# Kernel optimization log

Measured on AMD Instinct MI355X. Metric: run time of the kernel, lower is better.

The kernel has to match this reference:

```python
import jax, jax.numpy as jnp
import numpy as np

EPS = 1e-5
NUM_PIXELS = 2  # M_Relax window half-width


def _conv(x, w, b, groups=1, pad=0):
    y = jax.lax.conv_general_dilated(
        x, w, (1, 1), [(pad, pad), (pad, pad)],
        dimension_numbers=("NCHW", "OIHW", "NCHW"),
        feature_group_count=groups)
    return y + b[None, :, None, None]


def _bn(x, g, bta, m, v):
    # eval-mode BatchNorm2d with running stats
    inv = jax.lax.rsqrt(v + EPS)
    return g[None, :, None, None] * (x - m[None, :, None, None]) * inv[None, :, None, None] + bta[None, :, None, None]


def _resb(x, w1, b1, w2, b2):
    y = _conv(x, w1, b1, groups=4, pad=1)
    y = jnp.where(y > 0, y, 0.1 * y)  # LeakyReLU(0.1)
    y = _conv(y, w2, b2, groups=4, pad=1)
    return y + x


def _relax(M):
    # M: (N, w, w); sum of shifts +-NUM_PIXELS along the row (dim 1)
    w = M.shape[1]
    P = jnp.pad(M, ((0, 0), (NUM_PIXELS, NUM_PIXELS), (0, 0)))
    out = P[:, 0:w, :]
    for k in range(1, 2 * NUM_PIXELS + 1):
        out = out + P[:, k:k + w, :]
    return out


def setup_inputs() -> dict:
    key = jax.random.key(0)
    ks = jax.random.split(key, 16)
    b, c, h, w = 4, 64, 128, 256
    c2 = 2 * c
    s = 0.05
    inp = {
        "x_left": jax.random.normal(ks[0], (b, c, h, w), jnp.float32),
        "x_right": jax.random.normal(ks[1], (b, c, h, w), jnp.float32),
        "conv1_w": jax.random.normal(ks[2], (c, c, 1, 1), jnp.float32) * s,
        "conv1_b": jnp.zeros((c,), jnp.float32),
        "conv2_w": jax.random.normal(ks[3], (c, c, 1, 1), jnp.float32) * s,
        "conv2_b": jnp.zeros((c,), jnp.float32),
        "bn_g": jnp.ones((c2,), jnp.float32),
        "bn_b": jnp.zeros((c2,), jnp.float32),
        "bn_m": jax.random.normal(ks[4], (c2,), jnp.float32) * 0.1,
        "bn_v": jax.random.uniform(ks[5], (c2,), jnp.float32) + 0.5,
        "rb_w1": jax.random.normal(ks[6], (c2, c2 // 4, 3, 3), jnp.float32) * s,
        "rb_b1": jnp.zeros((c2,), jnp.float32),
        "rb_w2": jax.random.normal(ks[7], (c2, c2 // 4, 3, 3), jnp.float32) * s,
        "rb_b2": jnp.zeros((c2,), jnp.float32),
        "bq_w": jax.random.normal(ks[8], (c, c, 1, 1), jnp.float32) * s,
        "bq_b": jnp.zeros((c,), jnp.float32),
        "bs_w": jax.random.normal(ks[9], (c, c, 1, 1), jnp.float32) * s,
        "bs_b": jnp.zeros((c,), jnp.float32),
    }
    return inp


def reference(x_left, x_right, conv1_w, conv1_b, conv2_w, conv2_b,
              bn_g, bn_b, bn_m, bn_v, rb_w1, rb_b1, rb_w2, rb_b2,
              bq_w, bq_b, bs_w, bs_b):
    b, c, h, w = x_left.shape
    cat_l = jnp.concatenate([_conv(x_left, conv1_w, conv1_b), x_left], axis=1)
    cat_r = jnp.concatenate([_conv(x_right, conv2_w, conv2_b), x_right], axis=1)
    Q = _conv(_resb(_bn(cat_l, bn_g, bn_b, bn_m, bn_v), rb_w1, rb_b1, rb_w2, rb_b2), bq_w, bq_b, groups=2)
    K = _conv(_resb(_bn(cat_r, bn_g, bn_b, bn_m, bn_v), rb_w1, rb_b1, rb_w2, rb_b2), bs_w, bs_b, groups=2)
    Q = Q - Q.mean(axis=3, keepdims=True)
    K = K - K.mean(axis=3, keepdims=True)
    # score: (b*h, w, w) -- per-epipolar-row cross-view attention
    Qr = Q.transpose(0, 2, 3, 1).reshape(b * h, w, c)
    Kr = K.transpose(0, 2, 1, 3).reshape(b * h, c, w)
    score = jnp.matmul(Qr, Kr)
    M_r2l = jax.nn.softmax(score, axis=-1)
    M_l2r = jax.nn.softmax(score.transpose(0, 2, 1), axis=-1)
    # validity maps via relaxed cycle-consistency (detached in original)
    V_l = jnp.einsum("nij,nji->ni", _relax(M_r2l), M_l2r)
    V_r = jnp.einsum("nij,nji->ni", _relax(M_l2r), M_r2l)
    V_l = jax.lax.stop_gradient(V_l).reshape(b, 1, h, w)
    V_r = jax.lax.stop_gradient(V_r).reshape(b, 1, h, w)
    V_l_t = jnp.tanh(5.0 * V_l)
    V_r_t = jnp.tanh(5.0 * V_r)
    xl = x_left.transpose(0, 2, 3, 1).reshape(b * h, w, c)
    xr = x_right.transpose(0, 2, 3, 1).reshape(b * h, w, c)
    x_lT = jnp.matmul(M_r2l, xr).reshape(b, h, w, c).transpose(0, 3, 1, 2)
    x_rT = jnp.matmul(M_l2r, xl).reshape(b, h, w, c).transpose(0, 3, 1, 2)
    out_left = x_left * (1.0 - V_l_t) + x_lT * V_l_t
    out_right = x_right * (1.0 - V_r_t) + x_rT * V_r_t
    return out_left, out_right
```

## Files before the change

kernel.cpp:

```cpp
#include <hip/hip_runtime.h>
#include <math.h>

#define BB 4
#define CC 64
#define C2 128
#define HH 128
#define WW 256
#define NN (BB*HH)
#define EPSBN 1e-5f

typedef _Float16 f16;
typedef _Float16 half8 __attribute__((ext_vector_type(8)));
typedef float f32x4 __attribute__((ext_vector_type(4)));

__global__ __launch_bounds__(256) void k_wprep(
    const float* __restrict__ w1, const float* __restrict__ w2,
    f16* __restrict__ wp1, f16* __restrict__ wp2)
{
    int g = blockIdx.x; int which = blockIdx.y;
    const float* src = which ? w2 : w1;
    f16* dst = which ? wp2 : wp1;
    for (int p = threadIdx.x; p < 9216; p += 256) {
        int mo = p / 288; int kr = p - mo*288;
        int ks = kr >> 5; int ic = kr & 31;
        dst[g*9216 + p] = (f16)src[((g*32 + mo)*32 + ic)*9 + ks];
    }
}

__global__ __launch_bounds__(256) void k_catbn_m(
    const float* __restrict__ x, const float* __restrict__ cw, const float* __restrict__ cb,
    const float* __restrict__ g, const float* __restrict__ bb_, const float* __restrict__ m,
    const float* __restrict__ v, f16* __restrict__ u)
{
    __shared__ f16 Xl[256][72];
    __shared__ f16 Wl[64][72];
    __shared__ float sS[64], sT[64], sS2[64], sT2[64];
    int n = blockIdx.x; int b = n >> 7; int h = n & 127; int t = threadIdx.x;
    for (int p = t; p < 2048; p += 256) {
        int idx = p * 2; int o = idx >> 6, i = idx & 63;
        union { f16 h[2]; unsigned int u1; } pr;
        pr.h[0] = (f16)cw[idx]; pr.h[1] = (f16)cw[idx + 1];
        *(unsigned int*)&Wl[o][i] = pr.u1;
    }
    if (t < 64) {
        float inv = rsqrtf(v[t] + EPSBN); float s = g[t] * inv;
        sS[t] = s; sT[t] = bb_[t] + s * (cb[t] - m[t]);
        float inv2 = rsqrtf(v[t + 64] + EPSBN); float s2 = g[t + 64] * inv2;
        sS2[t] = s2; sT2[t] = bb_[t + 64] - s2 * m[t + 64];
    }
    __syncthreads();
    f16* up = u + ((size_t)(n*256 + t)) * 128;
    for (int c8 = 0; c8 < 8; ++c8) {
        float xv8[8];
#pragma unroll
        for (int j = 0; j < 8; ++j)
            xv8[j] = x[(((b*64 + c8*8 + j)*128 + h) << 8) + t];
        union { f16 h[8]; uint4 v4; } pk;
#pragma unroll
        for (int j = 0; j < 8; ++j) {
            int c = c8*8 + j;
            pk.h[j] = (f16)(sS2[c]*xv8[j] + sT2[c]);
        }
        *(uint4*)(up + 64 + c8*8) = pk.v4;
#pragma unroll
        for (int j2 = 0; j2 < 4; ++j2) {
            union { f16 h[2]; unsigned int u1; } q;
            q.h[0] = (f16)xv8[j2*2]; q.h[1] = (f16)xv8[j2*2 + 1];
            *(unsigned int*)&Xl[t][c8*8 + j2*2] = q.u1;
        }
    }
    __syncthreads();
    int lane = t & 63, wv = t >> 6;
    int m16 = lane & 15, quad = lane >> 4;
    half8 af[4][2], bf[4][2];
#pragma unroll
    for (int mt = 0; mt < 4; ++mt)
#pragma unroll
        for (int kk = 0; kk < 2; ++kk)
            af[mt][kk] = *(const half8*)&Wl[mt*16 + m16][kk*32 + quad*8];
#pragma unroll
    for (int nt = 0; nt < 4; ++nt)
#pragma unroll
        for (int kk = 0; kk < 2; ++kk)
            bf[nt][kk] = *(const half8*)&Xl[wv*64 + nt*16 + m16][kk*32 + quad*8];
    f32x4 acc[4][4] = {};
#pragma unroll
    for (int mt = 0; mt < 4; ++mt)
#pragma unroll
        for (int nt = 0; nt < 4; ++nt) {
            acc[mt][nt] = __builtin_amdgcn_mfma_f32_16x16x32_f16(af[mt][0], bf[nt][0], acc[mt][nt], 0, 0, 0);
            acc[mt][nt] = __builtin_amdgcn_mfma_f32_16x16x32_f16(af[mt][1], bf[nt][1], acc[mt][nt], 0, 0, 0);
        }
#pragma unroll
    for (int mt = 0; mt < 4; ++mt) {
        int ocb = mt*16 + quad*4;
        float s4[4], t4[4];
        *(float4*)s4 = *(const float4*)&sS[ocb];
        *(float4*)t4 = *(const float4*)&sT[ocb];
#pragma unroll
        for (int nt = 0; nt < 4; ++nt) {
            int px = wv*64 + nt*16 + m16;
            union { f16 h[4]; uint2 u2; } ov;
#pragma unroll
            for (int r = 0; r < 4; ++r)
                ov.h[r] = (f16)(s4[r]*acc[mt][nt][r] + t4[r]);
            *(uint2*)(u + ((size_t)(n*256 + px))*128 + ocb) = ov.u2;
        }
    }
}

template<bool LEAKY, bool RES>
__global__ __launch_bounds__(256, 2) void k_conv3r(
    const f16* __restrict__ in, const f16* __restrict__ wp,
    const float* __restrict__ bias, const f16* __restrict__ res,
    f16* __restrict__ out)
{
    __shared__ f16 Xl[6*130*40];
    int b = blockIdx.x >> 5; int h0 = (blockIdx.x & 31) * 4;
    int g = blockIdx.y; int w0 = blockIdx.z * 128;
    int t = threadIdx.x;
    int lane = t & 63, wv = t >> 6;
    int m16 = lane & 15, quad = lane >> 4;
    const f16* wg = wp + g*9216;
    half8 af[2][9];
#pragma unroll
    for (int mt = 0; mt < 2; ++mt)
#pragma unroll
        for (int ks = 0; ks < 9; ++ks)
            af[mt][ks] = *(const half8*)(wg + (mt*16 + m16)*288 + ks*32 + quad*8);
    float bo[2][4];
#pragma unroll
    for (int mt = 0; mt < 2; ++mt)
#pragma unroll
        for (int r = 0; r < 4; ++r)
            bo[mt][r] = bias[g*32 + mt*16 + quad*4 + r];
    for (int idx = t; idx < 3120; idx += 256) {
        int r = idx / 520; int rem = idx - r*520; int p = rem >> 2; int q = rem & 3;
        int hr = h0 + r - 1; int wg2 = w0 + p - 1;
        uint4 val = make_uint4(0,0,0,0);
        if ((unsigned)wg2 < 256u && (unsigned)hr < 128u)
            val = *(const uint4*)(in + ((size_t)((b*128 + hr)*256 + wg2))*128 + g*32 + q*8);
        *(uint4*)&Xl[(r*130 + p)*40 + q*8] = val;
    }
    __syncthreads();
    int px0 = wv*32 + m16;
#pragma unroll
    for (int rr = 0; rr < 4; ++rr) {
        f32x4 acc[2][2] = {};
#pragma unroll
        for (int ks = 0; ks < 9; ++ks) {
            int ky = ks / 3, kx = ks - ky*3;
            half8 bf0 = *(const half8*)&Xl[((rr + ky)*130 + px0 + kx)*40 + quad*8];
            half8 bf1 = *(const half8*)&Xl[((rr + ky)*130 + px0 + 16 + kx)*40 + quad*8];
            acc[0][0] = __builtin_amdgcn_mfma_f32_16x16x32_f16(af[0][ks], bf0, acc[0][0], 0, 0, 0);
            acc[0][1] = __builtin_amdgcn_mfma_f32_16x16x32_f16(af[0][ks], bf1, acc[0][1], 0, 0, 0);
            acc[1][0] = __builtin_amdgcn_mfma_f32_16x16x32_f16(af[1][ks], bf0, acc[1][0], 0, 0, 0);
            acc[1][1] = __builtin_amdgcn_mfma_f32_16x16x32_f16(af[1][ks], bf1, acc[1][1], 0, 0, 0);
        }
        int h = h0 + rr;
#pragma unroll
        for (int mt = 0; mt < 2; ++mt)
#pragma unroll
            for (int nt = 0; nt < 2; ++nt) {
                int px = w0 + wv*32 + nt*16 + m16;
                int oc = g*32 + mt*16 + quad*4;
                size_t off = ((size_t)((b*128 + h)*256 + px))*128 + oc;
                float rv4[4] = {0.f, 0.f, 0.f, 0.f};
                if (RES) {
                    union { f16 h[4]; uint2 v2; } rrd;
                    rrd.v2 = *(const uint2*)(res + off);
#pragma unroll
                    for (int r = 0; r < 4; ++r) rv4[r] = (float)rrd.h[r];
                }
                union { f16 h[4]; uint2 v2; } ov;
#pragma unroll
                for (int r = 0; r < 4; ++r) {
                    float y = acc[mt][nt][r] + bo[mt][r];
                    if (LEAKY) y = y > 0.f ? y : 0.1f*y;
                    if (RES) y += rv4[r];
                    ov.h[r] = (f16)y;
                }
                *(uint2*)(out + off) = ov.v2;
            }
    }
}

__global__ __launch_bounds__(256, 2) void k_conv1x1m(
    const f16* __restrict__ in, const float* __restrict__ wgt,
    f16* __restrict__ outq)
{
    __shared__ f16 Xl[256][72];
    __shared__ f16 Wl[64][72];
    __shared__ float partial[4][64];
    __shared__ float meanS[64];
    int n = blockIdx.x; int t = threadIdx.x;
    int lane = t & 63, wv = t >> 6;
    int m16 = lane & 15, quad = lane >> 4;
    for (int p = t; p < 2048; p += 256) {
        int idx = p * 2; int o = idx >> 6, i = idx & 63;
        union { f16 h[2]; unsigned int u1; } pr;
        pr.h[0] = (f16)wgt[idx]; pr.h[1] = (f16)wgt[idx + 1];
        *(unsigned int*)&Wl[o][i] = pr.u1;
    }
    f32x4 acc[4][4] = {};
    const f16* rp = in + ((size_t)n*256 + t)*128;
    for (int g = 0; g < 2; ++g) {
#pragma unroll
        for (int i8 = 0; i8 < 8; ++i8)
            *(uint4*)&Xl[t][i8*8] = *(const uint4*)(rp + g*64 + i8*8);
        __syncthreads();
        half8 af[2][2], bf[4][2];
#pragma unroll
        for (int ml = 0; ml < 2; ++ml)
#pragma unroll
            for (int kk = 0; kk < 2; ++kk)
                af[ml][kk] = *(const half8*)&Wl[g*32 + ml*16 + m16][kk*32 + quad*8];
#pragma unroll
        for (int nt = 0; nt < 4; ++nt)
#pragma unroll
            for (int kk = 0; kk < 2; ++kk)
                bf[nt][kk] = *(const half8*)&Xl[wv*64 + nt*16 + m16][kk*32 + quad*8];
#pragma unroll
        for (int ml = 0; ml < 2; ++ml)
#pragma unroll
            for (int nt = 0; nt < 4; ++nt) {
                int mt = g*2 + ml;
                acc[mt][nt] = __builtin_amdgcn_mfma_f32_16x16x32_f16(af[ml][0], bf[nt][0], acc[mt][nt], 0, 0, 0);
                acc[mt][nt] = __builtin_amdgcn_mfma_f32_16x16x32_f16(af[ml][1], bf[nt][1], acc[mt][nt], 0, 0, 0);
            }
        __syncthreads();
    }
#pragma unroll
    for (int mt = 0; mt < 4; ++mt)
#pragma unroll
        for (int r = 0; r < 4; ++r) {
            float s = acc[mt][0][r] + acc[mt][1][r] + acc[mt][2][r] + acc[mt][3][r];
            s += __shfl_xor(s, 1); s += __shfl_xor(s, 2);
            s += __shfl_xor(s, 4); s += __shfl_xor(s, 8);
            if (m16 == 0) partial[wv][mt*16 + quad*4 + r] = s;
        }
    __syncthreads();
    if (t < 64)
        meanS[t] = (partial[0][t] + partial[1][t] + partial[2][t] + partial[3][t]) * (1.0f/256.0f);
    __syncthreads();
    f16* qp = outq + ((size_t)n*256)*64;
#pragma unroll
    for (int mt = 0; mt < 4; ++mt) {
        int ocb = mt*16 + quad*4;
        float m4[4]; *(float4*)m4 = *(const float4*)&meanS[ocb];
#pragma unroll
        for (int nt = 0; nt < 4; ++nt) {
            int px = wv*64 + nt*16 + m16;
            union { f16 h[4]; uint2 u2; } ov;
#pragma unroll
            for (int r = 0; r < 4; ++r)
                ov.h[r] = (f16)(acc[mt][nt][r] - m4[r]);
            *(uint2*)(qp + (size_t)px*64 + ocb) = ov.u2;
        }
    }
}


template<int RIGHT>
__device__ __forceinline__ void attn_pass(
    const char* Sl, char* pool,
    const float* __restrict__ myM, const float* __restrict__ myI,
    const float* __restrict__ oM,  const float* __restrict__ oI,
    const float* __restrict__ xB, const float* __restrict__ xP,
    float* __restrict__ outp, int b, int h, int t)
{
    f16 (*Pl)[40] = (f16(*)[40])pool;
    f16 (*Xl)[40] = (f16(*)[40])(pool + 20800);
    float* scr = (float*)(pool + 20800);
    float* Vv  = (float*)(pool + 22848);
    int lane = t & 63, wv = t >> 6;
    int m16 = lane & 15, quad = lane >> 4;
    int W = wv * 32;
    int r = t & 255, hc = t >> 8;
    int cbase = hc * 16;
    float rm = myM[r], ri = myI[r];
    int xc = t >> 3, xj = (t & 7) * 4;
    const float* xg = xB + ((size_t)(b*64 + xc)*128 + h)*256;
    f32x4 acc[2][4] = {};
    float vacc = 0.f;
    const char* sb = Sl + (r << 9);
    int xo = (r & 7) << 4;
    for (int kc = 0; kc < 256; kc += 32) {
        float sraw[16];
        if (!RIGHT) {
            half8 v0 = *(const half8*)(sb + (((kc + cbase)*2)      ^ xo));
            half8 v1 = *(const half8*)(sb + (((kc + cbase)*2 + 16) ^ xo));
#pragma unroll
            for (int e = 0; e < 8; ++e) { sraw[e] = (float)v0[e]; sraw[8+e] = (float)v1[e]; }
        } else {
#pragma unroll
            for (int e = 0; e < 16; ++e) {
                int j = kc + cbase + e;
                sraw[e] = (float)*(const f16*)(Sl + (j << 9) + ((r*2) ^ ((j & 7) << 4)));
            }
        }
        {
            half8 p0, p1;
#pragma unroll
            for (int e = 0; e < 8; ++e) p0[e] = (f16)(__expf(sraw[e]     - rm) * ri);
#pragma unroll
            for (int e = 0; e < 8; ++e) p1[e] = (f16)(__expf(sraw[8 + e] - rm) * ri);
            char* pb = (char*)&Pl[r + 2][cbase];
            *(half8*)pb = p0; *(half8*)(pb + 16) = p1;
        }
        {
            float4 x4 = *(const float4*)(xg + kc + xj);
            union { f16 h[4]; uint2 v2; } px;
            px.h[0] = (f16)x4.x; px.h[1] = (f16)x4.y;
            px.h[2] = (f16)x4.z; px.h[3] = (f16)x4.w;
            *(uint2*)&Xl[xc][xj] = px.v2;
        }
        __syncthreads();
#pragma unroll
        for (int j8 = 0; j8 < 2; ++j8) {
            const char* wb = (const char*)&Pl[r][cbase + j8*8];
            half8 w0 = *(const half8*)(wb);
            half8 w1 = *(const half8*)(wb + 80);
            half8 w2 = *(const half8*)(wb + 160);
            half8 w3 = *(const half8*)(wb + 240);
            half8 w4 = *(const half8*)(wb + 320);
            half8 win = w0 + w1 + w2 + w3 + w4;
#pragma unroll
            for (int e = 0; e < 8; ++e) {
                int j = kc + cbase + j8*8 + e;
                float Bv = __expf(sraw[j8*8 + e] - oM[j]) * oI[j];
                vacc = fmaf((float)win[e], Bv, vacc);
            }
        }
        half8 pa[2], xb_[4];
#pragma unroll
        for (int mt = 0; mt < 2; ++mt)
            pa[mt] = *(const half8*)((const char*)&Pl[W + mt*16 + m16 + 2][0] + quad*16);
#pragma unroll
        for (int nt = 0; nt < 4; ++nt)
            xb_[nt] = *(const half8*)((const char*)&Xl[nt*16 + m16][0] + quad*16);
#pragma unroll
        for (int mt = 0; mt < 2; ++mt)
#pragma unroll
            for (int nt = 0; nt < 4; ++nt)
                acc[mt][nt] = __builtin_amdgcn_mfma_f32_16x16x32_f16(pa[mt], xb_[nt], acc[mt][nt], 0, 0, 0);
        __syncthreads();
    }
    scr[hc*256 + r] = vacc;
    __syncthreads();
    if (t < 256) Vv[t] = scr[t] + scr[256 + t];
    __syncthreads();
#pragma unroll
    for (int mt = 0; mt < 2; ++mt) {
        int i0 = W + mt*16 + quad*4;
        float v4[4];
        *(float4*)v4 = *(const float4*)&Vv[i0];
        float tv[4];
#pragma unroll
        for (int rr = 0; rr < 4; ++rr) tv[rr] = tanhf(5.f*v4[rr]);
#pragma unroll
        for (int nt = 0; nt < 4; ++nt) {
            int c = nt*16 + m16;
            size_t base = (((size_t)(b*64 + c)*128 + h) << 8) + i0;
            float xp4[4]; *(float4*)xp4 = *(const float4*)&xP[base];
            float o4[4];
#pragma unroll
            for (int rr = 0; rr < 4; ++rr)
                o4[rr] = xp4[rr]*(1.f - tv[rr]) + acc[mt][nt][rr]*tv[rr];
            *(float4*)&outp[base] = *(float4*)o4;
        }
    }
}

__global__ __launch_bounds__(512, 1) void k_attn2(
    const f16* __restrict__ Q, const f16* __restrict__ K,
    const float* __restrict__ xl, const float* __restrict__ xr,
    float* __restrict__ outL, float* __restrict__ outR)
{
    __shared__ f16 Sl[65536];
    __shared__ __align__(16) char pool[25920];
    __shared__ float rmS[256], riS[256], cmS[256], ciS[256];
    float* colM = (float*)pool;
    float* colS = (float*)(pool + 8192);
    int n = blockIdx.x; int b = n >> 7; int h = n & 127;
    int t = threadIdx.x;
    int lane = t & 63, wv = t >> 6;
    int m16 = lane & 15, quad = lane >> 4;
    int W = wv * 32;

    const f16* ag = Q + (size_t)n*16384;
    const f16* bg = K + (size_t)n*16384;
    half8 af1[2][2];
#pragma unroll
    for (int mt = 0; mt < 2; ++mt)
#pragma unroll
        for (int kk = 0; kk < 2; ++kk)
            af1[mt][kk] = *(const half8*)(ag + (size_t)(W + mt*16 + m16)*64 + kk*32 + quad*8);
    float rowm[8], rows_[8];
#pragma unroll
    for (int i = 0; i < 8; ++i) { rowm[i] = -1e30f; rows_[i] = 0.f; }
    for (int jc = 0; jc < 256; jc += 64) {
        half8 bf1[4][2];
#pragma unroll
        for (int nt = 0; nt < 4; ++nt)
#pragma unroll
            for (int kk = 0; kk < 2; ++kk)
                bf1[nt][kk] = *(const half8*)(bg + (size_t)(jc + nt*16 + m16)*64 + kk*32 + quad*8);
        f32x4 acc1[2][4] = {};
#pragma unroll
        for (int mt = 0; mt < 2; ++mt)
#pragma unroll
            for (int nt = 0; nt < 4; ++nt) {
                acc1[mt][nt] = __builtin_amdgcn_mfma_f32_16x16x32_f16(af1[mt][0], bf1[nt][0], acc1[mt][nt], 0, 0, 0);
                acc1[mt][nt] = __builtin_amdgcn_mfma_f32_16x16x32_f16(af1[mt][1], bf1[nt][1], acc1[mt][nt], 0, 0, 0);
            }
#pragma unroll
        for (int mt = 0; mt < 2; ++mt)
#pragma unroll
            for (int nt = 0; nt < 4; ++nt)
#pragma unroll
                for (int r = 0; r < 4; ++r) {
                    int row = W + mt*16 + quad*4 + r;
                    int col = jc + nt*16 + m16;
                    f16 hv = (f16)acc1[mt][nt][r];
                    *(f16*)((char*)Sl + (row << 9) + ((col*2) ^ ((row & 7) << 4))) = hv;
                    acc1[mt][nt][r] = (float)hv;
                }
#pragma unroll
        for (int mt = 0; mt < 2; ++mt)
#pragma unroll
            for (int r = 0; r < 4; ++r) {
                float lm = fmaxf(fmaxf(acc1[mt][0][r], acc1[mt][1][r]),
                                 fmaxf(acc1[mt][2][r], acc1[mt][3][r]));
                lm = fmaxf(lm, __shfl_xor(lm, 1));
                lm = fmaxf(lm, __shfl_xor(lm, 2));
                lm = fmaxf(lm, __shfl_xor(lm, 4));
                lm = fmaxf(lm, __shfl_xor(lm, 8));
                float le = __expf(acc1[mt][0][r] - lm) + __expf(acc1[mt][1][r] - lm)
                         + __expf(acc1[mt][2][r] - lm) + __expf(acc1[mt][3][r] - lm);
                le += __shfl_xor(le, 1); le += __shfl_xor(le, 2);
                le += __shfl_xor(le, 4); le += __shfl_xor(le, 8);
                int idx = mt*4 + r;
                float nm = fmaxf(rowm[idx], lm);
                rows_[idx] = rows_[idx]*__expf(rowm[idx] - nm) + le*__expf(lm - nm);
                rowm[idx] = nm;
            }
#pragma unroll
        for (int nt = 0; nt < 4; ++nt) {
            float lm = acc1[0][nt][0];
#pragma unroll
            for (int r = 1; r < 4; ++r) lm = fmaxf(lm, acc1[0][nt][r]);
#pragma unroll
            for (int r = 0; r < 4; ++r) lm = fmaxf(lm, acc1[1][nt][r]);
            lm = fmaxf(lm, __shfl_xor(lm, 16));
            lm = fmaxf(lm, __shfl_xor(lm, 32));
            float le = 0.f;
#pragma unroll
            for (int mt2 = 0; mt2 < 2; ++mt2)
#pragma unroll
                for (int r = 0; r < 4; ++r) le += __expf(acc1[mt2][nt][r] - lm);
            le += __shfl_xor(le, 16); le += __shfl_xor(le, 32);
            if (quad == 0) {
                int col = jc + nt*16 + m16;
                colM[wv*256 + col] = lm;
                colS[wv*256 + col] = le;
            }
        }
    }
    if (m16 == 0) {
#pragma unroll
        for (int mt = 0; mt < 2; ++mt)
#pragma unroll
            for (int r = 0; r < 4; ++r) {
                int row = W + mt*16 + quad*4 + r;
                rmS[row] = rowm[mt*4 + r];
                riS[row] = 1.0f / rows_[mt*4 + r];
            }
    }
    __syncthreads();
    if (t < 256) {
        float m = colM[t], s = colS[t];
#pragma unroll
        for (int w = 1; w < 8; ++w) {
            float m2 = colM[w*256 + t], s2 = colS[w*256 + t];
            float nm = fmaxf(m, m2);
            s = s*__expf(m - nm) + s2*__expf(m2 - nm);
            m = nm;
        }
        cmS[t] = m; ciS[t] = 1.0f / s;
    }
    __syncthreads();
    if (t < 10)       *(uint4*)(pool + t*16)           = make_uint4(0,0,0,0);
    else if (t < 20)  *(uint4*)(pool + 20640 + (t-10)*16) = make_uint4(0,0,0,0);

    attn_pass<0>((const char*)Sl, pool, rmS, riS, cmS, ciS, xr, xl, outL, b, h, t);
    __syncthreads();
    attn_pass<1>((const char*)Sl, pool, cmS, ciS, rmS, riS, xl, xr, outR, b, h, t);
}

extern "C" void kernel_launch(void* const* d_in, const int* in_sizes, int n_in,
                              void* d_out, int out_size, void* d_ws, size_t ws_size,
                              hipStream_t stream)
{
    const float* x_left  = (const float*)d_in[0];
    const float* x_right = (const float*)d_in[1];
    const float* conv1_w = (const float*)d_in[2];
    const float* conv1_b = (const float*)d_in[3];
    const float* conv2_w = (const float*)d_in[4];
    const float* conv2_b = (const float*)d_in[5];
    const float* bn_g    = (const float*)d_in[6];
    const float* bn_b    = (const float*)d_in[7];
    const float* bn_m    = (const float*)d_in[8];
    const float* bn_v    = (const float*)d_in[9];
    const float* rb_w1   = (const float*)d_in[10];
    const float* rb_b1   = (const float*)d_in[11];
    const float* rb_w2   = (const float*)d_in[12];
    const float* rb_b2   = (const float*)d_in[13];
    const float* bq_w    = (const float*)d_in[14];
    const float* bs_w    = (const float*)d_in[16];

    f16* W16 = (f16*)d_ws;
    f16* u  = W16;
    f16* y1 = W16 + 16777216;
    f16* r  = W16 + 33554432;
    f16* Qh = W16 + 67108864;
    f16* Kh = W16 + 75497472;
    f16* Wp1 = W16 + 84934656;
    f16* Wp2 = W16 + 84971520;

    float* out_left  = (float*)d_out;
    float* out_right = (float*)d_out + 8388608;

    k_wprep<<<dim3(4, 2), 256, 0, stream>>>(rb_w1, rb_w2, Wp1, Wp2);

    k_catbn_m<<<NN, 256, 0, stream>>>(x_left, conv1_w, conv1_b, bn_g, bn_b, bn_m, bn_v, u);
    k_conv3r<true,  false><<<dim3(128, 4, 2), 256, 0, stream>>>(u, Wp1, rb_b1, nullptr, y1);
    k_conv3r<false, true ><<<dim3(128, 4, 2), 256, 0, stream>>>(y1, Wp2, rb_b2, u, r);
    k_conv1x1m<<<NN, 256, 0, stream>>>(r, bq_w, Qh);

    k_catbn_m<<<NN, 256, 0, stream>>>(x_right, conv2_w, conv2_b, bn_g, bn_b, bn_m, bn_v, u);
    k_conv3r<true,  false><<<dim3(128, 4, 2), 256, 0, stream>>>(u, Wp1, rb_b1, nullptr, y1);
    k_conv3r<false, true ><<<dim3(128, 4, 2), 256, 0, stream>>>(y1, Wp2, rb_b2, u, r);
    k_conv1x1m<<<NN, 256, 0, stream>>>(r, bs_w, Kh);

    k_attn2<<<NN, 512, 0, stream>>>(Qh, Kh, x_left, x_right, out_left, out_right);
}
```

Before: 438.3 us.

## Double attention kernel block to 1024 threads with 16-row wave tiles

The fused attention kernel now runs 16 waves per block instead of 8, so each wave owns 16 rows of the score matrix and each thread handles 8 columns per chunk. Column softmax partials are kept in registers and merged pairwise through shared memory, and the reductions in the attention pass are rewritten for four-way column splits. The aim is more latency hiding and parallelism per CU, since the block already used most of the LDS and ran one block per CU. The cost is extra synchronisation and smaller MFMA tiles per wave, with less reuse of operands within a wave.

After: 442.1 us. About the same (+0.9%).

```diff
diff --git a/kernel.cpp b/kernel.cpp
--- a/kernel.cpp
+++ b/kernel.cpp
@@ -260,7 +260,6 @@
     }
 }
 
-
 template<int RIGHT>
 __device__ __forceinline__ void attn_pass(
     const char* Sl, char* pool,
@@ -272,53 +271,47 @@
     f16 (*Pl)[40] = (f16(*)[40])pool;
     f16 (*Xl)[40] = (f16(*)[40])(pool + 20800);
     float* scr = (float*)(pool + 20800);
-    float* Vv  = (float*)(pool + 22848);
+    float* Vv  = (float*)(pool + 24896);
     int lane = t & 63, wv = t >> 6;
     int m16 = lane & 15, quad = lane >> 4;
-    int W = wv * 32;
-    int r = t & 255, hc = t >> 8;
-    int cbase = hc * 16;
+    int W = wv * 16;
+    int r = t & 255, qc = t >> 8;
+    int cbase = qc * 8;
     float rm = myM[r], ri = myI[r];
-    int xc = t >> 3, xj = (t & 7) * 4;
+    int xc = t >> 4, xj = (t & 15) * 2;
     const float* xg = xB + ((size_t)(b*64 + xc)*128 + h)*256;
-    f32x4 acc[2][4] = {};
+    f32x4 acc[4] = {};
     float vacc = 0.f;
     const char* sb = Sl + (r << 9);
     int xo = (r & 7) << 4;
     for (int kc = 0; kc < 256; kc += 32) {
-        float sraw[16];
+        float sraw[8];
         if (!RIGHT) {
-            half8 v0 = *(const half8*)(sb + (((kc + cbase)*2)      ^ xo));
-            half8 v1 = *(const half8*)(sb + (((kc + cbase)*2 + 16) ^ xo));
-#pragma unroll
-            for (int e = 0; e < 8; ++e) { sraw[e] = (float)v0[e]; sraw[8+e] = (float)v1[e]; }
+            half8 v0 = *(const half8*)(sb + (((kc + cbase)*2) ^ xo));
+#pragma unroll
+            for (int e = 0; e < 8; ++e) sraw[e] = (float)v0[e];
         } else {
 #pragma unroll
-            for (int e = 0; e < 16; ++e) {
+            for (int e = 0; e < 8; ++e) {
                 int j = kc + cbase + e;
                 sraw[e] = (float)*(const f16*)(Sl + (j << 9) + ((r*2) ^ ((j & 7) << 4)));
             }
         }
         {
-            half8 p0, p1;
-#pragma unroll
-            for (int e = 0; e < 8; ++e) p0[e] = (f16)(__expf(sraw[e]     - rm) * ri);
-#pragma unroll
-            for (int e = 0; e < 8; ++e) p1[e] = (f16)(__expf(sraw[8 + e] - rm) * ri);
-            char* pb = (char*)&Pl[r + 2][cbase];
-            *(half8*)pb = p0; *(half8*)(pb + 16) = p1;
+            half8 p0;
+#pragma unroll
+            for (int e = 0; e < 8; ++e) p0[e] = (f16)(__expf(sraw[e] - rm) * ri);
+            *(half8*)&Pl[r + 2][cbase] = p0;
         }
         {
-            float4 x4 = *(const float4*)(xg + kc + xj);
-            union { f16 h[4]; uint2 v2; } px;
-            px.h[0] = (f16)x4.x; px.h[1] = (f16)x4.y;
-            px.h[2] = (f16)x4.z; px.h[3] = (f16)x4.w;
-            *(uint2*)&Xl[xc][xj] = px.v2;
+            float2 x2 = *(const float2*)(xg + kc + xj);
+            union { f16 h[2]; unsigned int u1; } px;
+            px.h[0] = (f16)x2.x; px.h[1] = (f16)x2.y;
+            *(unsigned int*)&Xl[xc][xj] = px.u1;
         }
         __syncthreads();
-#pragma unroll
-        for (int j8 = 0; j8 < 2; ++j8) {
-            const char* wb = (const char*)&Pl[r][cbase + j8*8];
+        {
+            const char* wb = (const char*)&Pl[r][cbase];
             half8 w0 = *(const half8*)(wb);
             half8 w1 = *(const half8*)(wb + 80);
             half8 w2 = *(const half8*)(wb + 160);
@@ -327,32 +320,27 @@
             half8 win = w0 + w1 + w2 + w3 + w4;
 #pragma unroll
             for (int e = 0; e < 8; ++e) {
-                int j = kc + cbase + j8*8 + e;
-                float Bv = __expf(sraw[j8*8 + e] - oM[j]) * oI[j];
+                int j = kc + cbase + e;
+                float Bv = __expf(sraw[e] - oM[j]) * oI[j];
                 vacc = fmaf((float)win[e], Bv, vacc);
             }
         }
-        half8 pa[2], xb_[4];
-#pragma unroll
-        for (int mt = 0; mt < 2; ++mt)
-            pa[mt] = *(const half8*)((const char*)&Pl[W + mt*16 + m16 + 2][0] + quad*16);
+        half8 pa = *(const half8*)((const char*)&Pl[W + m16 + 2][0] + quad*16);
+        half8 xb_[4];
 #pragma unroll
         for (int nt = 0; nt < 4; ++nt)
             xb_[nt] = *(const half8*)((const char*)&Xl[nt*16 + m16][0] + quad*16);
 #pragma unroll
-        for (int mt = 0; mt < 2; ++mt)
-#pragma unroll
-            for (int nt = 0; nt < 4; ++nt)
-                acc[mt][nt] = __builtin_amdgcn_mfma_f32_16x16x32_f16(pa[mt], xb_[nt], acc[mt][nt], 0, 0, 0);
+        for (int nt = 0; nt < 4; ++nt)
+            acc[nt] = __builtin_amdgcn_mfma_f32_16x16x32_f16(pa, xb_[nt], acc[nt], 0, 0, 0);
         __syncthreads();
     }
-    scr[hc*256 + r] = vacc;
-    __syncthreads();
-    if (t < 256) Vv[t] = scr[t] + scr[256 + t];
-    __syncthreads();
-#pragma unroll
-    for (int mt = 0; mt < 2; ++mt) {
-        int i0 = W + mt*16 + quad*4;
+    scr[qc*256 + r] = vacc;
+    __syncthreads();
+    if (t < 256) Vv[t] = scr[t] + scr[256 + t] + scr[512 + t] + scr[768 + t];
+    __syncthreads();
+    {
+        int i0 = W + quad*4;
         float v4[4];
         *(float4*)v4 = *(const float4*)&Vv[i0];
         float tv[4];
@@ -366,13 +354,13 @@
             float o4[4];
 #pragma unroll
             for (int rr = 0; rr < 4; ++rr)
-                o4[rr] = xp4[rr]*(1.f - tv[rr]) + acc[mt][nt][rr]*tv[rr];
+                o4[rr] = xp4[rr]*(1.f - tv[rr]) + acc[nt][rr]*tv[rr];
             *(float4*)&outp[base] = *(float4*)o4;
         }
     }
 }
 
-__global__ __launch_bounds__(512, 1) void k_attn2(
+__global__ __launch_bounds__(1024, 4) void k_attn2(
     const f16* __restrict__ Q, const f16* __restrict__ K,
     const float* __restrict__ xl, const float* __restrict__ xr,
     float* __restrict__ outL, float* __restrict__ outR)
@@ -386,95 +374,101 @@
     int t = threadIdx.x;
     int lane = t & 63, wv = t >> 6;
     int m16 = lane & 15, quad = lane >> 4;
-    int W = wv * 32;
+    int W = wv * 16;
 
     const f16* ag = Q + (size_t)n*16384;
     const f16* bg = K + (size_t)n*16384;
-    half8 af1[2][2];
-#pragma unroll
-    for (int mt = 0; mt < 2; ++mt)
-#pragma unroll
-        for (int kk = 0; kk < 2; ++kk)
-            af1[mt][kk] = *(const half8*)(ag + (size_t)(W + mt*16 + m16)*64 + kk*32 + quad*8);
-    float rowm[8], rows_[8];
-#pragma unroll
-    for (int i = 0; i < 8; ++i) { rowm[i] = -1e30f; rows_[i] = 0.f; }
-    for (int jc = 0; jc < 256; jc += 64) {
+    half8 af1[2];
+#pragma unroll
+    for (int kk = 0; kk < 2; ++kk)
+        af1[kk] = *(const half8*)(ag + (size_t)(W + m16)*64 + kk*32 + quad*8);
+    float rowm[4], rows_[4];
+#pragma unroll
+    for (int i = 0; i < 4; ++i) { rowm[i] = -1e30f; rows_[i] = 0.f; }
+    float cpm[16], cps[16];
+#pragma unroll
+    for (int jc4 = 0; jc4 < 4; ++jc4) {
+        int jc = jc4 * 64;
         half8 bf1[4][2];
 #pragma unroll
         for (int nt = 0; nt < 4; ++nt)
 #pragma unroll
             for (int kk = 0; kk < 2; ++kk)
                 bf1[nt][kk] = *(const half8*)(bg + (size_t)(jc + nt*16 + m16)*64 + kk*32 + quad*8);
-        f32x4 acc1[2][4] = {};
-#pragma unroll
-        for (int mt = 0; mt < 2; ++mt)
-#pragma unroll
-            for (int nt = 0; nt < 4; ++nt) {
-                acc1[mt][nt] = __builtin_amdgcn_mfma_f32_16x16x32_f16(af1[mt][0], bf1[nt][0], acc1[mt][nt], 0, 0, 0);
-                acc1[mt][nt] = __builtin_amdgcn_mfma_f32_16x16x32_f16(af1[mt][1], bf1[nt][1], acc1[mt][nt], 0, 0, 0);
-            }
-#pragma unroll
-        for (int mt = 0; mt < 2; ++mt)
-#pragma unroll
-            for (int nt = 0; nt < 4; ++nt)
-#pragma unroll
-                for (int r = 0; r < 4; ++r) {
-                    int row = W + mt*16 + quad*4 + r;
-                    int col = jc + nt*16 + m16;
-                    f16 hv = (f16)acc1[mt][nt][r];
-                    *(f16*)((char*)Sl + (row << 9) + ((col*2) ^ ((row & 7) << 4))) = hv;
-                    acc1[mt][nt][r] = (float)hv;
-                }
-#pragma unroll
-        for (int mt = 0; mt < 2; ++mt)
+        f32x4 acc1[4] = {};
+#pragma unroll
+        for (int nt = 0; nt < 4; ++nt) {
+            acc1[nt] = __builtin_amdgcn_mfma_f32_16x16x32_f16(af1[0], bf1[nt][0], acc1[nt], 0, 0, 0);
+            acc1[nt] = __builtin_amdgcn_mfma_f32_16x16x32_f16(af1[1], bf1[nt][1], acc1[nt], 0, 0, 0);
+        }
+#pragma unroll
+        for (int nt = 0; nt < 4; ++nt)
 #pragma unroll
             for (int r = 0; r < 4; ++r) {
-                float lm = fmaxf(fmaxf(acc1[mt][0][r], acc1[mt][1][r]),
-                                 fmaxf(acc1[mt][2][r], acc1[mt][3][r]));
-                lm = fmaxf(lm, __shfl_xor(lm, 1));
-                lm = fmaxf(lm, __shfl_xor(lm, 2));
-                lm = fmaxf(lm, __shfl_xor(lm, 4));
-                lm = fmaxf(lm, __shfl_xor(lm, 8));
-                float le = __expf(acc1[mt][0][r] - lm) + __expf(acc1[mt][1][r] - lm)
-                         + __expf(acc1[mt][2][r] - lm) + __expf(acc1[mt][3][r] - lm);
-                le += __shfl_xor(le, 1); le += __shfl_xor(le, 2);
-                le += __shfl_xor(le, 4); le += __shfl_xor(le, 8);
-                int idx = mt*4 + r;
-                float nm = fmaxf(rowm[idx], lm);
-                rows_[idx] = rows_[idx]*__expf(rowm[idx] - nm) + le*__expf(lm - nm);
-                rowm[idx] = nm;
-            }
+                int row = W + quad*4 + r;
+                int col = jc + nt*16 + m16;
+                f16 hv = (f16)acc1[nt][r];
+                *(f16*)((char*)Sl + (row << 9) + ((col*2) ^ ((row & 7) << 4))) = hv;
+                acc1[nt][r] = (float)hv;
+            }
+#pragma unroll
+        for (int r = 0; r < 4; ++r) {
+            float lm = fmaxf(fmaxf(acc1[0][r], acc1[1][r]), fmaxf(acc1[2][r], acc1[3][r]));
+            lm = fmaxf(lm, __shfl_xor(lm, 1));
+            lm = fmaxf(lm, __shfl_xor(lm, 2));
+            lm = fmaxf(lm, __shfl_xor(lm, 4));
+            lm = fmaxf(lm, __shfl_xor(lm, 8));
+            float le = __expf(acc1[0][r] - lm) + __expf(acc1[1][r] - lm)
+                     + __expf(acc1[2][r] - lm) + __expf(acc1[3][r] - lm);
+            le += __shfl_xor(le, 1); le += __shfl_xor(le, 2);
+            le += __shfl_xor(le, 4); le += __shfl_xor(le, 8);
+            float nm = fmaxf(rowm[r], lm);
+            rows_[r] = rows_[r]*__expf(rowm[r] - nm) + le*__expf(lm - nm);
+            rowm[r] = nm;
+        }
 #pragma unroll
         for (int nt = 0; nt < 4; ++nt) {
-            float lm = acc1[0][nt][0];
-#pragma unroll
-            for (int r = 1; r < 4; ++r) lm = fmaxf(lm, acc1[0][nt][r]);
-#pragma unroll
-            for (int r = 0; r < 4; ++r) lm = fmaxf(lm, acc1[1][nt][r]);
+            float lm = fmaxf(fmaxf(acc1[nt][0], acc1[nt][1]), fmaxf(acc1[nt][2], acc1[nt][3]));
             lm = fmaxf(lm, __shfl_xor(lm, 16));
             lm = fmaxf(lm, __shfl_xor(lm, 32));
             float le = 0.f;
 #pragma unroll
-            for (int mt2 = 0; mt2 < 2; ++mt2)
-#pragma unroll
-                for (int r = 0; r < 4; ++r) le += __expf(acc1[mt2][nt][r] - lm);
+            for (int r = 0; r < 4; ++r) le += __expf(acc1[nt][r] - lm);
             le += __shfl_xor(le, 16); le += __shfl_xor(le, 32);
-            if (quad == 0) {
-                int col = jc + nt*16 + m16;
-                colM[wv*256 + col] = lm;
-                colS[wv*256 + col] = le;
-            }
+            cpm[jc4*4 + nt] = lm;
+            cps[jc4*4 + nt] = le;
         }
     }
     if (m16 == 0) {
 #pragma unroll
-        for (int mt = 0; mt < 2; ++mt)
-#pragma unroll
-            for (int r = 0; r < 4; ++r) {
-                int row = W + mt*16 + quad*4 + r;
-                rmS[row] = rowm[mt*4 + r];
-                riS[row] = 1.0f / rows_[mt*4 + r];
+        for (int r = 0; r < 4; ++r) {
+            int row = W + quad*4 + r;
+            rmS[row] = rowm[r];
+            riS[row] = 1.0f / rows_[r];
+        }
+    }
+    if (wv >= 8 && quad == 0) {
+#pragma unroll
+        for (int jc4 = 0; jc4 < 4; ++jc4)
+#pragma unroll
+            for (int nt = 0; nt < 4; ++nt) {
+                int col = jc4*64 + nt*16 + m16;
+                colM[(wv - 8)*256 + col] = cpm[jc4*4 + nt];
+                colS[(wv - 8)*256 + col] = cps[jc4*4 + nt];
+            }
+    }
+    __syncthreads();
+    if (wv < 8 && quad == 0) {
+#pragma unroll
+        for (int jc4 = 0; jc4 < 4; ++jc4)
+#pragma unroll
+            for (int nt = 0; nt < 4; ++nt) {
+                int col = jc4*64 + nt*16 + m16;
+                float m1 = cpm[jc4*4 + nt], s1 = cps[jc4*4 + nt];
+                float m2 = colM[wv*256 + col], s2 = colS[wv*256 + col];
+                float nm = fmaxf(m1, m2);
+                colM[wv*256 + col] = nm;
+                colS[wv*256 + col] = s1*__expf(m1 - nm) + s2*__expf(m2 - nm);
             }
     }
     __syncthreads();
@@ -490,7 +484,7 @@
         cmS[t] = m; ciS[t] = 1.0f / s;
     }
     __syncthreads();
-    if (t < 10)       *(uint4*)(pool + t*16)           = make_uint4(0,0,0,0);
+    if (t < 10)       *(uint4*)(pool + t*16)              = make_uint4(0,0,0,0);
     else if (t < 20)  *(uint4*)(pool + 20640 + (t-10)*16) = make_uint4(0,0,0,0);
 
     attn_pass<0>((const char*)Sl, pool, rmS, riS, cmS, ciS, xr, xl, outL, b, h, t);
@@ -543,5 +537,5 @@
     k_conv3r<false, true ><<<dim3(128, 4, 2), 256, 0, stream>>>(y1, Wp2, rb_b2, u, r);
     k_conv1x1m<<<NN, 256, 0, stream>>>(r, bs_w, Kh);
 
-    k_attn2<<<NN, 512, 0, stream>>>(Qh, Kh, x_left, x_right, out_left, out_right);
-}
+    k_attn2<<<NN, 1024, 0, stream>>>(Qh, Kh, x_left, x_right, out_left, out_right);
+}
```
